# Performance work log

Hardware: AMD Instinct MI355X
Metric: run time of the kernel (lower is better)

## Reference

```python
import jax, jax.numpy as jnp
import numpy as np

B, C, H, Wd = 16, 512, 56, 56
WCH = 128  # W_ch: projection rank of phi/rou


def setup_inputs() -> dict:
    key = jax.random.key(0)
    ks = jax.random.split(key, 8)
    s = 0.02
    return {
        "x": jax.random.normal(ks[0], (B, C, H, Wd), dtype=jnp.float32),
        "y": jax.random.normal(ks[1], (B, C, H, Wd), dtype=jnp.float32),
        # phi: Conv2d(C, WCH, 1) -> weight [WCH, C], bias [WCH]
        "phi_w": jax.random.normal(ks[2], (WCH, C), dtype=jnp.float32) * s,
        "phi_b": jnp.zeros((WCH,), dtype=jnp.float32),
        # rou: Conv2d(C, WCH, 1) applied to globally pooled y -> acts as Linear
        "rou_w": jax.random.normal(ks[3], (WCH, C), dtype=jnp.float32) * s,
        "rou_b": jnp.zeros((WCH,), dtype=jnp.float32),
        # zeta: Linear(C, C)
        "zeta_w": jax.random.normal(ks[4], (C, C), dtype=jnp.float32) * s,
        "zeta_b": jnp.zeros((C,), dtype=jnp.float32),
    }


def reference(x, y, phi_w, phi_b, rou_w, rou_b, zeta_w, zeta_b):
    b, c, h, w = x.shape
    hw = h * w
    # phi_xT = relu(phi(x)).view(B, WCH, HW); phi_x = transpose -> [B, HW, WCH]
    phi_xT = jax.nn.relu(jnp.einsum('kc,bchw->bkhw', phi_w, x) + phi_b[None, :, None, None])
    phi_x = phi_xT.reshape(b, -1, hw).transpose(0, 2, 1)  # [B, HW, WCH]
    # rou_y = sigmoid(rou(global_avg_pool(y))) -> [B, WCH]
    pooled = y.mean(axis=(2, 3))  # [B, C]
    rou_y = jax.nn.sigmoid(pooled @ rou_w.T + rou_b)  # [B, WCH]
    # D_i = sum_j (phi_x diag(rou) phi_x^T)_{ij} = sum_k phi_x[i,k] rou[k] s[k]
    s = phi_x.sum(axis=1)  # [B, WCH], column sums
    D = jnp.einsum('bnk,bk,bk->bn', phi_x, rou_y, s)  # [B, HW]
    inv_sqrt = 1.0 / jnp.sqrt(D + 1e-8)
    P = phi_x * inv_sqrt[..., None]  # diag(D^-1/2) @ phi_x, [B, HW, WCH]
    # x.view(B, -1, C): raw row-major reshape of [B,C,H,W] (NOT a transpose)
    x_trans = x.reshape(b, hw, c)
    # LX = x_trans - P diag(rou) P^T x_trans, re-associated right-to-left
    t = jnp.einsum('bnk,bnc->bkc', P, x_trans)          # P^T x_trans, [B, WCH, C]
    LX = x_trans - jnp.einsum('bnk,bk,bkc->bnc', P, rou_y, t)
    # zeta Linear + dropout(eval: identity) + relu, residual add
    out = jax.nn.relu(LX @ zeta_w.T + zeta_b)
    return x + out.reshape(b, c, h, w)
```

## Files before the change

kernel.cpp:

```cpp
#include <hip/hip_runtime.h>
#include <math.h>

#define B_  16
#define C_  512
#define HW_ 3136
#define K_  128
#define CHW (C_ * HW_)

typedef __bf16 bf16x8_t __attribute__((ext_vector_type(8)));
typedef __bf16 bf16x4_t __attribute__((ext_vector_type(4)));
typedef float floatx4  __attribute__((ext_vector_type(4)));

typedef const __attribute__((address_space(1))) void* gas_ptr;
typedef __attribute__((address_space(3))) void*       las_ptr;

static __device__ __forceinline__ unsigned short bfbits(__bf16 v) {
    return __builtin_bit_cast(unsigned short, v);
}

__device__ __forceinline__ void stage128x64(const __bf16* __restrict__ base, long ld,
                                            int row0, int rowmax, int k0,
                                            __bf16* lds, int t) {
    int w = t >> 6;
    #pragma unroll
    for (int i = 0; i < 4; ++i) {
        int u = i * 256 + t;
        int m = u >> 3, slot = u & 7;
        int kg = slot ^ (m & 7);
        int r = row0 + m; if (r > rowmax) r = rowmax;
        const __bf16* g = base + (long)r * ld + (k0 + kg * 8);
        __bf16* l = lds + (size_t)(i * 256 + w * 64) * 8;
        __builtin_amdgcn_global_load_lds((gas_ptr)g, (las_ptr)l, 16, 0, 0);
    }
}

__device__ __forceinline__ void stage_tr(const __bf16* __restrict__ src, long ld,
                                         int r0, int p0, char* Bs, int t) {
    int rg = t & 15;
    int pp2 = (t >> 4) * 2;
    #pragma unroll
    for (int ci = 0; ci < 2; ++ci) {
        int cc = pp2 + ci * 32;
        const __bf16* g0 = src + (long)(p0 + cc) * ld + r0 + rg * 8;
        bf16x8_t v0 = *(const bf16x8_t*)g0;
        bf16x8_t v1 = *(const bf16x8_t*)(g0 + ld);
        int r8 = cc >> 3, sub = (cc & 7) >> 1;
        #pragma unroll
        for (int j = 0; j < 8; ++j) {
            int row = rg * 8 + j;
            int slot = (r8 + row + (row >> 3)) & 7;
            unsigned int pr = ((unsigned int)bfbits(v1[j]) << 16) | bfbits(v0[j]);
            *(unsigned int*)(Bs + row * 144 + slot * 16 + sub * 4) = pr;
        }
    }
}

__device__ __forceinline__ void mma_step64(const char* As, const char* Bs,
                                           floatx4 acc[4][4], int aoff, int boff,
                                           int q, int lxor) {
    #pragma unroll
    for (int h = 0; h < 2; ++h) {
        int s = (((h * 4 + q) ^ lxor) << 4);
        bf16x8_t af[4], bf[4];
        #pragma unroll
        for (int i = 0; i < 4; ++i) af[i] = *(const bf16x8_t*)(As + aoff + i * 2048 + s);
        #pragma unroll
        for (int i = 0; i < 4; ++i) bf[i] = *(const bf16x8_t*)(Bs + boff + i * 2048 + s);
        #pragma unroll
        for (int mi = 0; mi < 4; ++mi)
            #pragma unroll
            for (int ni = 0; ni < 4; ++ni)
                acc[mi][ni] = __builtin_amdgcn_mfma_f32_16x16x32_bf16(af[mi], bf[ni], acc[mi][ni], 0, 0, 0);
    }
}

__device__ __forceinline__ void mma_step_mix(const char* As, const char* Bs,
                                             floatx4 acc[4][4], int lm, int q,
                                             int wrow, int wcol) {
    int lxor = lm & 7;
    int aoff = (wrow * 64 + lm) * 128;
    #pragma unroll
    for (int h = 0; h < 2; ++h) {
        int g = h * 4 + q;
        int sa = (g ^ lxor) << 4;
        bf16x8_t af[4], bf[4];
        #pragma unroll
        for (int i = 0; i < 4; ++i) af[i] = *(const bf16x8_t*)(As + aoff + i * 2048 + sa);
        #pragma unroll
        for (int i = 0; i < 4; ++i) {
            int brow = wcol * 64 + i * 16 + lm;
            int slot = (g + brow + (brow >> 3)) & 7;
            bf[i] = *(const bf16x8_t*)(Bs + brow * 144 + slot * 16);
        }
        #pragma unroll
        for (int mi = 0; mi < 4; ++mi)
            #pragma unroll
            for (int ni = 0; ni < 4; ++ni)
                acc[mi][ni] = __builtin_amdgcn_mfma_f32_16x16x32_bf16(af[mi], bf[ni], acc[mi][ni], 0, 0, 0);
    }
}

__device__ __forceinline__ void mma_step_rot2(const char* As, const char* Bs,
                                              floatx4 acc[4][4], int lm, int q,
                                              int wrow, int wcol) {
    #pragma unroll
    for (int h = 0; h < 2; ++h) {
        int g = h * 4 + q;
        bf16x8_t af[4], bf[4];
        #pragma unroll
        for (int i = 0; i < 4; ++i) {
            int arow = wrow * 64 + i * 16 + lm;
            int aslot = (g + arow + (arow >> 3)) & 7;
            af[i] = *(const bf16x8_t*)(As + arow * 144 + aslot * 16);
        }
        #pragma unroll
        for (int i = 0; i < 4; ++i) {
            int brow = wcol * 64 + i * 16 + lm;
            int bslot = (g + brow + (brow >> 3)) & 7;
            bf[i] = *(const bf16x8_t*)(Bs + brow * 144 + bslot * 16);
        }
        #pragma unroll
        for (int mi = 0; mi < 4; ++mi)
            #pragma unroll
            for (int ni = 0; ni < 4; ++ni)
                acc[mi][ni] = __builtin_amdgcn_mfma_f32_16x16x32_bf16(af[mi], bf[ni], acc[mi][ni], 0, 0, 0);
    }
}


__global__ __launch_bounds__(256) void k_pool(const float* __restrict__ y,
                                              float* __restrict__ pooled) {
    int bc = blockIdx.x;
    const float* yp = y + (long)bc * HW_;
    int t = threadIdx.x;
    float acc = 0.f;
    #pragma unroll
    for (int i = 0; i < 4; ++i) {
        int n4 = t + i * 256;
        if (n4 < 784) {
            float4 v = *reinterpret_cast<const float4*>(yp + (long)n4 * 4);
            acc += v.x + v.y + v.z + v.w;
        }
    }
    #pragma unroll
    for (int off = 32; off > 0; off >>= 1) acc += __shfl_xor(acc, off, 64);
    __shared__ float red[4];
    if ((t & 63) == 0) red[t >> 6] = acc;
    __syncthreads();
    if (t == 0) pooled[bc] = (red[0] + red[1] + red[2] + red[3]) * (1.0f / HW_);
}

__global__ __launch_bounds__(64) void k_rou(const float* __restrict__ pooled,
                                            const float* __restrict__ rou_w,
                                            const float* __restrict__ rou_b,
                                            float* __restrict__ rou_y) {
    int k = blockIdx.x;
    int b = blockIdx.y;
    int lane = threadIdx.x;
    const float* pr = pooled + b * C_;
    const float* wr = rou_w + (long)k * C_;
    float acc = 0.f;
    #pragma unroll
    for (int i = 0; i < 2; ++i) {
        int c = (lane + i * 64) * 4;
        float4 w4 = *reinterpret_cast<const float4*>(wr + c);
        float4 p4 = *reinterpret_cast<const float4*>(pr + c);
        acc += w4.x * p4.x + w4.y * p4.y + w4.z * p4.z + w4.w * p4.w;
    }
    #pragma unroll
    for (int off = 32; off > 0; off >>= 1) acc += __shfl_xor(acc, off, 64);
    if (lane == 0) rou_y[b * K_ + k] = 1.0f / (1.0f + expf(-(acc + rou_b[k])));
}

__global__ __launch_bounds__(256) void k_cast8(const float* __restrict__ a,
                                               __bf16* __restrict__ o) {
    long i = ((long)blockIdx.x * 256 + threadIdx.x) * 8;
    float4 v0 = *reinterpret_cast<const float4*>(a + i);
    float4 v1 = *reinterpret_cast<const float4*>(a + i + 4);
    bf16x8_t r;
    r[0] = (__bf16)v0.x; r[1] = (__bf16)v0.y; r[2] = (__bf16)v0.z; r[3] = (__bf16)v0.w;
    r[4] = (__bf16)v1.x; r[5] = (__bf16)v1.y; r[6] = (__bf16)v1.z; r[7] = (__bf16)v1.w;
    *reinterpret_cast<bf16x8_t*>(o + i) = r;
}


__global__ __launch_bounds__(256) void k_phi_m(const __bf16* __restrict__ xbf2,
                                               const __bf16* __restrict__ pwbf,
                                               const float* __restrict__ phi_b,
                                               __bf16* __restrict__ phi_nk,
                                               float* __restrict__ sbuf) {
    int b = blockIdx.y;
    int n0 = blockIdx.x * 128;
    __shared__ __attribute__((aligned(16))) char smem[2 * 34816];
    int t = threadIdx.x, w = t >> 6, lane = t & 63;
    int lm = lane & 15, q = lane >> 4;
    int wrow = w >> 1, wcol = w & 1;
    floatx4 acc[4][4];
    #pragma unroll
    for (int i = 0; i < 4; ++i)
        #pragma unroll
        for (int j = 0; j < 4; ++j) acc[i][j] = (floatx4){0.f, 0.f, 0.f, 0.f};

    const __bf16* Bb = xbf2 + (long)b * CHW;

    stage128x64(pwbf, C_, 0, K_ - 1, 0, (__bf16*)smem, t);
    stage_tr(Bb, HW_, n0, 0, smem + 16384, t);
    __syncthreads();
    int cur = 0;
    #pragma unroll
    for (int s = 0; s < 8; ++s) {
        char* cb = smem + cur * 34816;
        if (s < 7) {
            char* nb = smem + (cur ^ 1) * 34816;
            int p0 = (s + 1) * 64;
            stage128x64(pwbf, C_, 0, K_ - 1, p0, (__bf16*)nb, t);
            stage_tr(Bb, HW_, n0, p0, nb + 16384, t);
        }
        mma_step_mix(cb, cb + 16384, acc, lm, q, wrow, wcol);
        __syncthreads();
        cur ^= 1;
    }
    #pragma unroll
    for (int mi = 0; mi < 4; ++mi) {
        int kb = wrow * 64 + mi * 16 + q * 4;
        float4 pb = *reinterpret_cast<const float4*>(phi_b + kb);
        float pbv[4] = {pb.x, pb.y, pb.z, pb.w};
        float sv[4] = {0.f, 0.f, 0.f, 0.f};
        #pragma unroll
        for (int ni = 0; ni < 4; ++ni) {
            int n = n0 + wcol * 64 + ni * 16 + lm;
            if (n < HW_) {
                bf16x4_t pack;
                #pragma unroll
                for (int r = 0; r < 4; ++r) {
                    float v = fmaxf(acc[mi][ni][r] + pbv[r], 0.f);
                    pack[r] = (__bf16)v;
                    sv[r] += v;
                }
                *reinterpret_cast<bf16x4_t*>(phi_nk + ((long)b * HW_ + n) * K_ + kb) = pack;
            }
        }
        #pragma unroll
        for (int r = 0; r < 4; ++r) {
            float v = sv[r];
            v += __shfl_xor(v, 1, 64); v += __shfl_xor(v, 2, 64);
            v += __shfl_xor(v, 4, 64); v += __shfl_xor(v, 8, 64);
            if (lm == 0) atomicAdd(&sbuf[b * K_ + kb + r], v);
        }
    }
}

__global__ __launch_bounds__(256) void k_d2(__bf16* __restrict__ phi_nk,
                                            const float* __restrict__ rou_y,
                                            const float* __restrict__ s,
                                            float* __restrict__ inv_s) {
    int b = blockIdx.y;
    __shared__ float ws[K_];
    int t = threadIdx.x;
    if (t < K_) ws[t] = rou_y[b * K_ + t] * s[b * K_ + t];
    __syncthreads();
    int w = t >> 6, lane = t & 63;
    int sub = lane >> 4, lm = lane & 15;
    int n = blockIdx.x * 16 + w * 4 + sub;
    __bf16* p = phi_nk + ((long)b * HW_ + n) * K_ + lm * 8;
    bf16x8_t v = *reinterpret_cast<bf16x8_t*>(p);
    float f[8];
    #pragma unroll
    for (int j = 0; j < 8; ++j) f[j] = (float)v[j];
    float d = 0.f;
    #pragma unroll
    for (int j = 0; j < 8; ++j) d += f[j] * ws[lm * 8 + j];
    d += __shfl_xor(d, 1, 64); d += __shfl_xor(d, 2, 64);
    d += __shfl_xor(d, 4, 64); d += __shfl_xor(d, 8, 64);
    float inv = rsqrtf(d + 1e-8f);
    bf16x8_t o;
    #pragma unroll
    for (int j = 0; j < 8; ++j) o[j] = (__bf16)(f[j] * inv);
    *reinterpret_cast<bf16x8_t*>(p) = o;
    if (lm == 0) inv_s[b * HW_ + n] = inv;
}

__global__ __launch_bounds__(256) void k_t_m(const __bf16* __restrict__ pnk,
                                             const __bf16* __restrict__ xbf2,
                                             float* __restrict__ t_part) {
    int gid = blockIdx.x;
    int rlo = gid & 7, cc4 = (gid >> 3) & 3, r8 = gid >> 5;
    int r = r8 * 8 + rlo;
    int b = r / 7, nch = r % 7;
    int c0 = cc4 * 128;
    __shared__ __attribute__((aligned(16))) char smem[2 * 36864];
    int t = threadIdx.x, w = t >> 6, lane = t & 63;
    int lm = lane & 15, q = lane >> 4;
    int wrow = w >> 1, wcol = w & 1;
    floatx4 acc[4][4];
    #pragma unroll
    for (int i = 0; i < 4; ++i)
        #pragma unroll
        for (int j = 0; j < 4; ++j) acc[i][j] = (floatx4){0.f, 0.f, 0.f, 0.f};

    const __bf16* Ab = pnk + (long)b * (long)HW_ * K_;
    const __bf16* Bb = xbf2 + (long)b * CHW;

    int pstart = nch * 448;
    stage_tr(Ab, K_, 0, pstart, smem, t);
    stage_tr(Bb, C_, c0, pstart, smem + 18432, t);
    __syncthreads();
    int cur = 0;
    #pragma unroll
    for (int s = 0; s < 7; ++s) {
        char* cb = smem + cur * 36864;
        if (s < 6) {
            char* nb = smem + (cur ^ 1) * 36864;
            int p0 = pstart + (s + 1) * 64;
            stage_tr(Ab, K_, 0, p0, nb, t);
            stage_tr(Bb, C_, c0, p0, nb + 18432, t);
        }
        mma_step_rot2(cb, cb + 18432, acc, lm, q, wrow, wcol);
        __syncthreads();
        cur ^= 1;
    }
    float* outp = t_part + ((long)nch * B_ + b) * K_ * C_;
    #pragma unroll
    for (int mi = 0; mi < 4; ++mi) {
        int kb = wrow * 64 + mi * 16 + q * 4;
        #pragma unroll
        for (int ni = 0; ni < 4; ++ni) {
            int c = c0 + wcol * 64 + ni * 16 + lm;
            #pragma unroll
            for (int rr = 0; rr < 4; ++rr)
                outp[(long)(kb + rr) * C_ + c] = acc[mi][ni][rr];
        }
    }
}

__global__ __launch_bounds__(256) void k_tred(const float* __restrict__ t_part,
                                              __bf16* __restrict__ t_bf) {
    const long BKC = (long)B_ * K_ * C_;
    long i = ((long)blockIdx.x * 256 + threadIdx.x) * 4;
    float4 s = *reinterpret_cast<const float4*>(t_part + i);
    #pragma unroll
    for (int p = 1; p < 7; ++p) {
        float4 v = *reinterpret_cast<const float4*>(t_part + p * BKC + i);
        s.x += v.x; s.y += v.y; s.z += v.z; s.w += v.w;
    }
    bf16x4_t o;
    o[0] = (__bf16)s.x; o[1] = (__bf16)s.y; o[2] = (__bf16)s.z; o[3] = (__bf16)s.w;
    *reinterpret_cast<bf16x4_t*>(t_bf + i) = o;
}

__global__ __launch_bounds__(256) void k_tz_m(const __bf16* __restrict__ zwbf,
                                              const __bf16* __restrict__ t_bf,
                                              const float* __restrict__ rou_y,
                                              __bf16* __restrict__ tzT) {
    int b = blockIdx.y;
    int c0 = blockIdx.x * 128;
    __shared__ __attribute__((aligned(16))) char smem[2 * 32768];
    int t = threadIdx.x, w = t >> 6, lane = t & 63;
    int lm = lane & 15, q = lane >> 4;
    int wrow = w >> 1, wcol = w & 1;
    floatx4 acc[4][4];
    #pragma unroll
    for (int i = 0; i < 4; ++i)
        #pragma unroll
        for (int j = 0; j < 4; ++j) acc[i][j] = (floatx4){0.f, 0.f, 0.f, 0.f};

    const __bf16* Bb = t_bf + (long)b * K_ * C_;
    int lxor = lm & 7;
    int aoff = (wrow * 64 + lm) * 128;
    int boff = (wcol * 64 + lm) * 128;

    stage128x64(zwbf, C_, c0, C_ - 1, 0, (__bf16*)smem, t);
    stage128x64(Bb,   C_, 0, K_ - 1, 0, (__bf16*)(smem + 16384), t);
    __syncthreads();
    int cur = 0;
    #pragma unroll
    for (int s = 0; s < 8; ++s) {
        char* cb = smem + cur * 32768;
        if (s < 7) {
            char* nb = smem + (cur ^ 1) * 32768;
            int p0 = (s + 1) * 64;
            stage128x64(zwbf, C_, c0, C_ - 1, p0, (__bf16*)nb, t);
            stage128x64(Bb,   C_, 0, K_ - 1, p0, (__bf16*)(nb + 16384), t);
        }
        mma_step64(cb, cb + 16384, acc, aoff, boff, q, lxor);
        __syncthreads();
        cur ^= 1;
    }
    #pragma unroll
    for (int mi = 0; mi < 4; ++mi) {
        int c = c0 + wrow * 64 + mi * 16 + q * 4;
        #pragma unroll
        for (int ni = 0; ni < 4; ++ni) {
            int k = wcol * 64 + ni * 16 + lm;
            float rk = rou_y[b * K_ + k];
            #pragma unroll
            for (int rr = 0; rr < 4; ++rr)
                tzT[((long)b * C_ + c + rr) * K_ + k] = (__bf16)(-rk * acc[mi][ni][rr]);
        }
    }
}

__global__ __launch_bounds__(256) void k_out_m(const __bf16* __restrict__ xbf2,
                                               const __bf16* __restrict__ zwbf,
                                               const __bf16* __restrict__ pnk,
                                               const __bf16* __restrict__ tzT,
                                               const float* __restrict__ zeta_b,
                                               float* __restrict__ out) {
    int gid = blockIdx.x;
    int rlo = gid & 7, cc4 = (gid >> 3) & 3, r8 = gid >> 5;
    int r = r8 * 8 + rlo;
    int b = r / 25, nt = r % 25;
    int n0 = nt * 128;
    int c0 = cc4 * 128;
    __shared__ __attribute__((aligned(16))) char smem[2 * 32768];
    int t = threadIdx.x, w = t >> 6, lane = t & 63;
    int lm = lane & 15, q = lane >> 4;
    int wrow = w >> 1, wcol = w & 1;
    floatx4 acc[4][4];
    #pragma unroll
    for (int i = 0; i < 4; ++i)
        #pragma unroll
        for (int j = 0; j < 4; ++j) acc[i][j] = (floatx4){0.f, 0.f, 0.f, 0.f};

    int lxor = lm & 7;
    int aoff = (wrow * 64 + lm) * 128;
    int boff = (wcol * 64 + lm) * 128;

    const __bf16* A1 = xbf2 + (long)b * CHW;
    const __bf16* A2 = pnk + (long)b * (long)HW_ * K_;
    const __bf16* B2 = tzT + (long)b * (long)C_ * K_;

    stage128x64(A1,   C_, n0, HW_ - 1, 0, (__bf16*)smem, t);
    stage128x64(zwbf, C_, c0, C_ - 1, 0, (__bf16*)(smem + 16384), t);
    __syncthreads();
    int cur = 0;
    #pragma unroll
    for (int s = 0; s < 10; ++s) {
        char* cb = smem + cur * 32768;
        if (s < 9) {
            char* nb = smem + (cur ^ 1) * 32768;
            int sn = s + 1;
            if (sn < 8) {
                int p0 = sn * 64;
                stage128x64(A1,   C_, n0, HW_ - 1, p0, (__bf16*)nb, t);
                stage128x64(zwbf, C_, c0, C_ - 1, p0, (__bf16*)(nb + 16384), t);
            } else {
                int p0 = (sn - 8) * 64;
                stage128x64(A2, K_, n0, HW_ - 1, p0, (__bf16*)nb, t);
                stage128x64(B2, K_, c0, C_ - 1, p0, (__bf16*)(nb + 16384), t);
            }
        }
        mma_step64(cb, cb + 16384, acc, aoff, boff, q, lxor);
        __syncthreads();
        cur ^= 1;
    }
    float* ep = (float*)smem;
    const __bf16* xres = xbf2 + (long)b * CHW;
    int lr = t >> 3, lc = (t & 7) * 16;
    #pragma unroll
    for (int ch = 0; ch < 4; ++ch) {
        __syncthreads();
        if (wrow == (ch >> 1)) {
            #pragma unroll
            for (int mm = 0; mm < 2; ++mm) {
                int mi = (ch & 1) * 2 + mm;
                #pragma unroll
                for (int ni = 0; ni < 4; ++ni)
                    #pragma unroll
                    for (int rr = 0; rr < 4; ++rr)
                        ep[(mm * 16 + q * 4 + rr) * 132 + wcol * 64 + ni * 16 + lm] = acc[mi][ni][rr];
            }
        }
        __syncthreads();
        int n = n0 + ch * 32 + lr;
        if (n < HW_) {
            long rowbase = (long)n * C_ + c0 + lc;
            bf16x8_t x0 = *(const bf16x8_t*)(xres + rowbase);
            bf16x8_t x1 = *(const bf16x8_t*)(xres + rowbase + 8);
            float xv[16];
            #pragma unroll
            for (int j = 0; j < 8; ++j) { xv[j] = (float)x0[j]; xv[8 + j] = (float)x1[j]; }
            float* orow = out + (long)b * CHW + rowbase;
            #pragma unroll
            for (int jj = 0; jj < 4; ++jj) {
                float4 zb = *reinterpret_cast<const float4*>(zeta_b + c0 + lc + jj * 4);
                float4 e  = *reinterpret_cast<const float4*>(&ep[lr * 132 + lc + jj * 4]);
                float4 o;
                o.x = xv[jj * 4 + 0] + fmaxf(e.x + zb.x, 0.f);
                o.y = xv[jj * 4 + 1] + fmaxf(e.y + zb.y, 0.f);
                o.z = xv[jj * 4 + 2] + fmaxf(e.z + zb.z, 0.f);
                o.w = xv[jj * 4 + 3] + fmaxf(e.w + zb.w, 0.f);
                *reinterpret_cast<float4*>(orow + jj * 4) = o;
            }
        }
    }
}

extern "C" void kernel_launch(void* const* d_in, const int* in_sizes, int n_in,
                              void* d_out, int out_size, void* d_ws, size_t ws_size,
                              hipStream_t stream) {
    const float* x      = (const float*)d_in[0];
    const float* y      = (const float*)d_in[1];
    const float* phi_w  = (const float*)d_in[2];
    const float* phi_b  = (const float*)d_in[3];
    const float* rou_w  = (const float*)d_in[4];
    const float* rou_b  = (const float*)d_in[5];
    const float* zeta_w = (const float*)d_in[6];
    const float* zeta_b = (const float*)d_in[7];
    float* out = (float*)d_out;

    char* p = (char*)d_ws;
    __bf16* xbf2   = (__bf16*)p; p += (size_t)B_ * CHW * 2;
    __bf16* phi_nk = (__bf16*)p; p += (size_t)B_ * K_ * HW_ * 2;
    float*  t_part = (float*) p; p += (size_t)7 * B_ * K_ * C_ * 4;
    __bf16* t_bf   = (__bf16*)p; p += (size_t)B_ * K_ * C_ * 2;
    __bf16* tzT    = (__bf16*)p; p += (size_t)B_ * C_ * K_ * 2;
    __bf16* pwbf   = (__bf16*)p; p += (size_t)K_ * C_ * 2;
    __bf16* zwbf   = (__bf16*)p; p += (size_t)C_ * C_ * 2;
    float*  pooled = (float*) p; p += (size_t)B_ * C_ * 4;
    float*  rou_y  = (float*) p; p += (size_t)B_ * K_ * 4;
    float*  sbuf   = (float*) p; p += (size_t)B_ * K_ * 4;
    float*  inv_s  = (float*) p; p += (size_t)B_ * HW_ * 4;

    hipMemsetAsync(sbuf, 0, B_ * K_ * sizeof(float), stream);

    k_pool <<<B_ * C_, 256, 0, stream>>>(y, pooled);
    k_rou  <<<dim3(K_, B_), 64, 0, stream>>>(pooled, rou_w, rou_b, rou_y);
    k_cast8<<<(K_ * C_) / 2048, 256, 0, stream>>>(phi_w, pwbf);
    k_cast8<<<(C_ * C_) / 2048, 256, 0, stream>>>(zeta_w, zwbf);
    k_cast8<<<(B_ * (long)CHW) / 2048, 256, 0, stream>>>(x, xbf2);
    k_phi_m<<<dim3(25, B_), 256, 0, stream>>>(xbf2, pwbf, phi_b, phi_nk, sbuf);
    k_d2   <<<dim3(HW_ / 16, B_), 256, 0, stream>>>(phi_nk, rou_y, sbuf, inv_s);
    k_t_m  <<<448, 256, 0, stream>>>(phi_nk, xbf2, t_part);
    k_tred <<<(B_ * K_ * C_) / 1024, 256, 0, stream>>>(t_part, t_bf);
    k_tz_m <<<dim3(C_ / 128, B_), 256, 0, stream>>>(zwbf, t_bf, rou_y, tzT);
    k_out_m<<<1600, 256, 0, stream>>>(xbf2, zwbf, phi_nk, tzT, zeta_b, out);
}
```

Before: 387.4 us.

## Fuse prep kernels, fold rou into phi GEMM, fold t-reduction into tz staging

Merges the three cast kernels, the pooling kernel and the sbuf memset into one k_prep launch. The rou sigmoid-linear is computed by the blockIdx.x==0 blocks of k_phi_m, and the 7-way partial-sum reduction of t is done while staging LDS tiles in k_tz_m, so k_tred and the t_bf buffer are dropped. This removes several launches and one intermediate round trip. In exchange, k_tz_m reads 7x fp32 partials per tile, and every C-tile block re-reads them, so the same partial sums are summed redundantly across blocks. It also uses synchronous loads in place of async LDS loads.

```diff
diff --git a/kernel.cpp b/kernel.cpp
--- a/kernel.cpp
+++ b/kernel.cpp
@@ -34,6 +34,32 @@
     }
 }
 
+__device__ __forceinline__ void stage_tsum(const float* __restrict__ tp, int p0,
+                                           char* lds, int t) {
+    const long BKC = (long)B_ * K_ * C_;
+    #pragma unroll
+    for (int i = 0; i < 4; ++i) {
+        int u = i * 256 + t;
+        int m = u >> 3, slot = u & 7;
+        int kg = slot ^ (m & 7);
+        const float* g = tp + (long)m * C_ + (p0 + kg * 8);
+        float4 a0 = *reinterpret_cast<const float4*>(g);
+        float4 a1 = *reinterpret_cast<const float4*>(g + 4);
+        #pragma unroll
+        for (int p = 1; p < 7; ++p) {
+            const float* gp = g + (long)p * BKC;
+            float4 v0 = *reinterpret_cast<const float4*>(gp);
+            float4 v1 = *reinterpret_cast<const float4*>(gp + 4);
+            a0.x += v0.x; a0.y += v0.y; a0.z += v0.z; a0.w += v0.w;
+            a1.x += v1.x; a1.y += v1.y; a1.z += v1.z; a1.w += v1.w;
+        }
+        bf16x8_t pk;
+        pk[0] = (__bf16)a0.x; pk[1] = (__bf16)a0.y; pk[2] = (__bf16)a0.z; pk[3] = (__bf16)a0.w;
+        pk[4] = (__bf16)a1.x; pk[5] = (__bf16)a1.y; pk[6] = (__bf16)a1.z; pk[7] = (__bf16)a1.w;
+        *reinterpret_cast<bf16x8_t*>(lds + (size_t)u * 16) = pk;
+    }
+}
+
 __device__ __forceinline__ void stage_tr(const __bf16* __restrict__ src, long ld,
                                          int r0, int p0, char* Bs, int t) {
     int rg = t & 15;
@@ -127,66 +153,60 @@
     }
 }
 
-
-__global__ __launch_bounds__(256) void k_pool(const float* __restrict__ y,
-                                              float* __restrict__ pooled) {
-    int bc = blockIdx.x;
-    const float* yp = y + (long)bc * HW_;
+__global__ __launch_bounds__(256) void k_prep(const float* __restrict__ x,
+                                              const float* __restrict__ y,
+                                              const float* __restrict__ phi_w,
+                                              const float* __restrict__ zeta_w,
+                                              __bf16* __restrict__ xbf2,
+                                              float* __restrict__ pooled,
+                                              __bf16* __restrict__ pwbf,
+                                              __bf16* __restrict__ zwbf,
+                                              float* __restrict__ sbuf) {
+    int gid = blockIdx.x;
     int t = threadIdx.x;
-    float acc = 0.f;
-    #pragma unroll
-    for (int i = 0; i < 4; ++i) {
-        int n4 = t + i * 256;
-        if (n4 < 784) {
-            float4 v = *reinterpret_cast<const float4*>(yp + (long)n4 * 4);
-            acc += v.x + v.y + v.z + v.w;
-        }
-    }
-    #pragma unroll
-    for (int off = 32; off > 0; off >>= 1) acc += __shfl_xor(acc, off, 64);
-    __shared__ float red[4];
-    if ((t & 63) == 0) red[t >> 6] = acc;
-    __syncthreads();
-    if (t == 0) pooled[bc] = (red[0] + red[1] + red[2] + red[3]) * (1.0f / HW_);
-}
-
-__global__ __launch_bounds__(64) void k_rou(const float* __restrict__ pooled,
-                                            const float* __restrict__ rou_w,
-                                            const float* __restrict__ rou_b,
-                                            float* __restrict__ rou_y) {
-    int k = blockIdx.x;
-    int b = blockIdx.y;
-    int lane = threadIdx.x;
-    const float* pr = pooled + b * C_;
-    const float* wr = rou_w + (long)k * C_;
-    float acc = 0.f;
-    #pragma unroll
-    for (int i = 0; i < 2; ++i) {
-        int c = (lane + i * 64) * 4;
-        float4 w4 = *reinterpret_cast<const float4*>(wr + c);
-        float4 p4 = *reinterpret_cast<const float4*>(pr + c);
-        acc += w4.x * p4.x + w4.y * p4.y + w4.z * p4.z + w4.w * p4.w;
-    }
-    #pragma unroll
-    for (int off = 32; off > 0; off >>= 1) acc += __shfl_xor(acc, off, 64);
-    if (lane == 0) rou_y[b * K_ + k] = 1.0f / (1.0f + expf(-(acc + rou_b[k])));
-}
-
-__global__ __launch_bounds__(256) void k_cast8(const float* __restrict__ a,
-                                               __bf16* __restrict__ o) {
-    long i = ((long)blockIdx.x * 256 + threadIdx.x) * 8;
-    float4 v0 = *reinterpret_cast<const float4*>(a + i);
-    float4 v1 = *reinterpret_cast<const float4*>(a + i + 4);
-    bf16x8_t r;
-    r[0] = (__bf16)v0.x; r[1] = (__bf16)v0.y; r[2] = (__bf16)v0.z; r[3] = (__bf16)v0.w;
-    r[4] = (__bf16)v1.x; r[5] = (__bf16)v1.y; r[6] = (__bf16)v1.z; r[7] = (__bf16)v1.w;
-    *reinterpret_cast<bf16x8_t*>(o + i) = r;
+    if (gid < 12704) {
+        const float* src; __bf16* dst; long off;
+        if (gid < 32)       { src = phi_w;  dst = pwbf; off = (long)gid * 2048; }
+        else if (gid < 160) { src = zeta_w; dst = zwbf; off = (long)(gid - 32) * 2048; }
+        else                { src = x;      dst = xbf2; off = (long)(gid - 160) * 2048; }
+        long i = off + (long)t * 8;
+        float4 v0 = *reinterpret_cast<const float4*>(src + i);
+        float4 v1 = *reinterpret_cast<const float4*>(src + i + 4);
+        bf16x8_t r;
+        r[0] = (__bf16)v0.x; r[1] = (__bf16)v0.y; r[2] = (__bf16)v0.z; r[3] = (__bf16)v0.w;
+        r[4] = (__bf16)v1.x; r[5] = (__bf16)v1.y; r[6] = (__bf16)v1.z; r[7] = (__bf16)v1.w;
+        *reinterpret_cast<bf16x8_t*>(dst + i) = r;
+    } else if (gid < 20896) {
+        int bc = gid - 12704;
+        const float* yp = y + (long)bc * HW_;
+        float acc = 0.f;
+        #pragma unroll
+        for (int i = 0; i < 4; ++i) {
+            int n4 = t + i * 256;
+            if (n4 < 784) {
+                float4 v = *reinterpret_cast<const float4*>(yp + (long)n4 * 4);
+                acc += v.x + v.y + v.z + v.w;
+            }
+        }
+        #pragma unroll
+        for (int off = 32; off > 0; off >>= 1) acc += __shfl_xor(acc, off, 64);
+        __shared__ float red[4];
+        if ((t & 63) == 0) red[t >> 6] = acc;
+        __syncthreads();
+        if (t == 0) pooled[bc] = (red[0] + red[1] + red[2] + red[3]) * (1.0f / HW_);
+    } else {
+        for (int i = t; i < B_ * K_; i += 256) sbuf[i] = 0.f;
+    }
 }
 
 
 __global__ __launch_bounds__(256) void k_phi_m(const __bf16* __restrict__ xbf2,
                                                const __bf16* __restrict__ pwbf,
                                                const float* __restrict__ phi_b,
+                                               const float* __restrict__ pooled,
+                                               const float* __restrict__ rou_w,
+                                               const float* __restrict__ rou_b,
+                                               float* __restrict__ rou_y,
                                                __bf16* __restrict__ phi_nk,
                                                float* __restrict__ sbuf) {
     int b = blockIdx.y;
@@ -195,6 +215,22 @@
     int t = threadIdx.x, w = t >> 6, lane = t & 63;
     int lm = lane & 15, q = lane >> 4;
     int wrow = w >> 1, wcol = w & 1;
+
+    if (blockIdx.x == 0) {
+        int k = t >> 1, h = t & 1;
+        const float* pr = pooled + b * C_ + h * 256;
+        const float* wr = rou_w + (long)k * C_ + h * 256;
+        float a = 0.f;
+        #pragma unroll 4
+        for (int c = 0; c < 256; c += 4) {
+            float4 w4 = *reinterpret_cast<const float4*>(wr + c);
+            float4 p4 = *reinterpret_cast<const float4*>(pr + c);
+            a += w4.x * p4.x + w4.y * p4.y + w4.z * p4.z + w4.w * p4.w;
+        }
+        a += __shfl_xor(a, 1, 64);
+        if (h == 0) rou_y[b * K_ + k] = 1.0f / (1.0f + expf(-(a + rou_b[k])));
+    }
+
     floatx4 acc[4][4];
     #pragma unroll
     for (int i = 0; i < 4; ++i)
@@ -333,23 +369,8 @@
     }
 }
 
-__global__ __launch_bounds__(256) void k_tred(const float* __restrict__ t_part,
-                                              __bf16* __restrict__ t_bf) {
-    const long BKC = (long)B_ * K_ * C_;
-    long i = ((long)blockIdx.x * 256 + threadIdx.x) * 4;
-    float4 s = *reinterpret_cast<const float4*>(t_part + i);
-    #pragma unroll
-    for (int p = 1; p < 7; ++p) {
-        float4 v = *reinterpret_cast<const float4*>(t_part + p * BKC + i);
-        s.x += v.x; s.y += v.y; s.z += v.z; s.w += v.w;
-    }
-    bf16x4_t o;
-    o[0] = (__bf16)s.x; o[1] = (__bf16)s.y; o[2] = (__bf16)s.z; o[3] = (__bf16)s.w;
-    *reinterpret_cast<bf16x4_t*>(t_bf + i) = o;
-}
-
 __global__ __launch_bounds__(256) void k_tz_m(const __bf16* __restrict__ zwbf,
-                                              const __bf16* __restrict__ t_bf,
+                                              const float* __restrict__ t_part,
                                               const float* __restrict__ rou_y,
                                               __bf16* __restrict__ tzT) {
     int b = blockIdx.y;
@@ -364,13 +385,13 @@
         #pragma unroll
         for (int j = 0; j < 4; ++j) acc[i][j] = (floatx4){0.f, 0.f, 0.f, 0.f};
 
-    const __bf16* Bb = t_bf + (long)b * K_ * C_;
+    const float* Tb = t_part + (long)b * K_ * C_;
     int lxor = lm & 7;
     int aoff = (wrow * 64 + lm) * 128;
     int boff = (wcol * 64 + lm) * 128;
 
     stage128x64(zwbf, C_, c0, C_ - 1, 0, (__bf16*)smem, t);
-    stage128x64(Bb,   C_, 0, K_ - 1, 0, (__bf16*)(smem + 16384), t);
+    stage_tsum(Tb, 0, smem + 16384, t);
     __syncthreads();
     int cur = 0;
     #pragma unroll
@@ -380,7 +401,7 @@
             char* nb = smem + (cur ^ 1) * 32768;
             int p0 = (s + 1) * 64;
             stage128x64(zwbf, C_, c0, C_ - 1, p0, (__bf16*)nb, t);
-            stage128x64(Bb,   C_, 0, K_ - 1, p0, (__bf16*)(nb + 16384), t);
+            stage_tsum(Tb, p0, nb + 16384, t);
         }
         mma_step64(cb, cb + 16384, acc, aoff, boff, q, lxor);
         __syncthreads();
@@ -513,7 +534,6 @@
     __bf16* xbf2   = (__bf16*)p; p += (size_t)B_ * CHW * 2;
     __bf16* phi_nk = (__bf16*)p; p += (size_t)B_ * K_ * HW_ * 2;
     float*  t_part = (float*) p; p += (size_t)7 * B_ * K_ * C_ * 4;
-    __bf16* t_bf   = (__bf16*)p; p += (size_t)B_ * K_ * C_ * 2;
     __bf16* tzT    = (__bf16*)p; p += (size_t)B_ * C_ * K_ * 2;
     __bf16* pwbf   = (__bf16*)p; p += (size_t)K_ * C_ * 2;
     __bf16* zwbf   = (__bf16*)p; p += (size_t)C_ * C_ * 2;
@@ -522,17 +542,11 @@
     float*  sbuf   = (float*) p; p += (size_t)B_ * K_ * 4;
     float*  inv_s  = (float*) p; p += (size_t)B_ * HW_ * 4;
 
-    hipMemsetAsync(sbuf, 0, B_ * K_ * sizeof(float), stream);
-
-    k_pool <<<B_ * C_, 256, 0, stream>>>(y, pooled);
-    k_rou  <<<dim3(K_, B_), 64, 0, stream>>>(pooled, rou_w, rou_b, rou_y);
-    k_cast8<<<(K_ * C_) / 2048, 256, 0, stream>>>(phi_w, pwbf);
-    k_cast8<<<(C_ * C_) / 2048, 256, 0, stream>>>(zeta_w, zwbf);
-    k_cast8<<<(B_ * (long)CHW) / 2048, 256, 0, stream>>>(x, xbf2);
-    k_phi_m<<<dim3(25, B_), 256, 0, stream>>>(xbf2, pwbf, phi_b, phi_nk, sbuf);
+    k_prep <<<20897, 256, 0, stream>>>(x, y, phi_w, zeta_w, xbf2, pooled, pwbf, zwbf, sbuf);
+    k_phi_m<<<dim3(25, B_), 256, 0, stream>>>(xbf2, pwbf, phi_b, pooled, rou_w, rou_b,
+                                              rou_y, phi_nk, sbuf);
     k_d2   <<<dim3(HW_ / 16, B_), 256, 0, stream>>>(phi_nk, rou_y, sbuf, inv_s);
     k_t_m  <<<448, 256, 0, stream>>>(phi_nk, xbf2, t_part);
-    k_tred <<<(B_ * K_ * C_) / 1024, 256, 0, stream>>>(t_part, t_bf);
-    k_tz_m <<<dim3(C_ / 128, B_), 256, 0, stream>>>(zwbf, t_bf, rou_y, tzT);
+    k_tz_m <<<dim3(C_ / 128, B_), 256, 0, stream>>>(zwbf, t_part, rou_y, tzT);
     k_out_m<<<1600, 256, 0, stream>>>(xbf2, zwbf, phi_nk, tzT, zeta_b, out);
 }
```

After: 402.2 us. 3.8% more time.
